# Performance work log

Hardware: AMD Instinct MI355X
Metric: run time of the kernel (lower is better)

## Reference

```python
import jax, jax.numpy as jnp
import numpy as np

N = 100000      # nodes
F_IN = 500      # num_features
H = 128         # num_hidden
C = 40          # num_classes
E = 3200000     # structural edges
K = 5           # knn neighbors


def setup_inputs() -> dict:
    key = jax.random.key(0)
    ks = jax.random.split(key, 9)
    x = jax.random.normal(ks[0], (N, F_IN), dtype=jnp.float32)
    edge_index = jax.random.randint(ks[1], (2, E), 0, N, dtype=jnp.int64)
    # knn graph: source i repeated K times, targets random (stand-in for cosine-KNN)
    src = jnp.repeat(jnp.arange(N, dtype=jnp.int64), K)
    dst = jax.random.randint(ks[2], (K * N,), 0, N, dtype=jnp.int64)
    edge_index_knn = jnp.stack([src, dst])
    s = lambda f: np.float32(1.0 / np.sqrt(f))
    W1 = jax.random.normal(ks[3], (F_IN, H), jnp.float32) * s(F_IN)
    b1 = jnp.zeros((H,), jnp.float32)
    W2 = jax.random.normal(ks[4], (2 * H, C), jnp.float32) * s(2 * H)
    b2 = jnp.zeros((C,), jnp.float32)
    Wlin = jax.random.normal(ks[5], (C, 2 * C), jnp.float32) * s(2 * C)  # torch Linear layout [out,in]
    blin = jnp.zeros((C,), jnp.float32)
    return {"x": x, "edge_index": edge_index, "edge_index_knn": edge_index_knn,
            "W1": W1, "b1": b1, "W2": W2, "b2": b2, "Wlin": Wlin, "blin": blin}


def gcn_conv(x, W, b, edge_index):
    # PyG GCNConv: add self-loops, symmetric normalization deg^-1/2 A deg^-1/2, x@W, scatter-add, +bias
    n = x.shape[0]
    loop = jnp.arange(n, dtype=edge_index.dtype)
    row = jnp.concatenate([edge_index[0], loop])  # sources (gathered)
    col = jnp.concatenate([edge_index[1], loop])  # targets (scattered)
    deg = jax.ops.segment_sum(jnp.ones_like(col, x.dtype), col, num_segments=n)
    dinv = jnp.where(deg > 0, jax.lax.rsqrt(jnp.maximum(deg, 1e-12)), 0.0).astype(x.dtype)
    norm = dinv[row] * dinv[col]                      # [E+n]
    h = x @ W                                          # [n, out]
    agg = jax.ops.segment_sum(h[row] * norm[:, None], col, num_segments=n)
    return agg + b


def reference(x, edge_index, edge_index_knn, W1, b1, W2, b2, Wlin, blin):
    h1 = gcn_conv(x, W1, b1, edge_index)
    h1_2 = gcn_conv(x, W1, b1, edge_index_knn)
    R1 = jax.nn.relu(jnp.concatenate([h1, h1_2], axis=1))  # dropout identity (eval mode)
    h2 = gcn_conv(R1, W2, b2, edge_index)
    h2_2 = gcn_conv(R1, W2, b2, edge_index_knn)
    R2 = jnp.concatenate([h2, h2_2], axis=1)
    logits = R2 @ Wlin.T + blin
    return jax.nn.log_softmax(logits, axis=1)
```

## Files before the change

### kernel.cpp

```cpp
#include <hip/hip_runtime.h>
#include <stdint.h>

#define NN   100000
#define FIN  500
#define HID  128
#define KP1  512
#define K2   256
#define CO   40
#define NPQ  80
#define NPQP 128
#define NBUCK 391
#define CAPB_S 9216
#define CAPB_K 1536

typedef __attribute__((ext_vector_type(8))) short short8;
typedef __attribute__((ext_vector_type(4))) float float4v;
typedef __attribute__((address_space(3))) unsigned int as3_u32;
typedef __attribute__((address_space(1))) unsigned int as1_u32;

__device__ __forceinline__ unsigned short f2bf(float f) {
  unsigned u = __float_as_uint(f);
  u = u + 0x7fffu + ((u >> 16) & 1u);
  return (unsigned short)(u >> 16);
}
__device__ __forceinline__ float bf2f(unsigned short s) {
  return __uint_as_float(((unsigned)s) << 16);
}
__device__ __forceinline__ void gl_lds16(const void* g, void* l) {
  __builtin_amdgcn_global_load_lds((const as1_u32*)g, (as3_u32*)l, 16, 0, 0);
}

__global__ __launch_bounds__(256) void k_bin(
    const int* __restrict__ ei, int nS, int nb1S, int* __restrict__ gcur_s, int* __restrict__ gbin_s,
    const int* __restrict__ eik, int nK, int* __restrict__ gcur_k, int* __restrict__ gbin_k) {
  __shared__ int cnt[NBUCK];
  __shared__ int base[NBUCK];
  const int b = blockIdx.x;
  const bool knn = (b >= nb1S);
  const int* src = knn ? eik      : ei;
  const int* tgt = knn ? eik + nK : ei + nS;
  const int n    = knn ? nK : nS;
  int* gcur      = knn ? gcur_k : gcur_s;
  int* gbin      = knn ? gbin_k : gbin_s;
  const int capb = knn ? CAPB_K : CAPB_S;
  const int ebase = (knn ? b - nb1S : b) * 4096;
  const int t = threadIdx.x;

  for (int i = t; i < NBUCK; i += 256) cnt[i] = 0;
  __syncthreads();
  int s[16], g[16];
#pragma unroll
  for (int i = 0; i < 16; ++i) {
    const int e = ebase + i * 256 + t;
    const bool v = e < n;
    s[i] = v ? src[e] : 0;
    g[i] = v ? tgt[e] : -1;
    if (v) atomicAdd(&cnt[g[i] >> 8], 1);
  }
  __syncthreads();
  for (int i = t; i < NBUCK; i += 256) {
    const int c = cnt[i];
    base[i] = c ? atomicAdd(&gcur[i], c) : 0;
    cnt[i] = 0;
  }
  __syncthreads();
#pragma unroll
  for (int i = 0; i < 16; ++i) {
    if (g[i] >= 0) {
      const int bkt = g[i] >> 8;
      const int pos = base[bkt] + atomicAdd(&cnt[bkt], 1);
      if (pos < capb) gbin[bkt * capb + pos] = (s[i] << 8) | (g[i] & 255);
    }
  }
}

__global__ __launch_bounds__(512) void k_bscan(const int* __restrict__ gcur_s, int* __restrict__ bscan_s,
                                               const int* __restrict__ gcur_k, int* __restrict__ bscan_k) {
  __shared__ int sd[512];
  const int* gcur = blockIdx.x ? gcur_k : gcur_s;
  int* bscan      = blockIdx.x ? bscan_k : bscan_s;
  const int t = threadIdx.x;
  const int v = (t < NBUCK) ? gcur[t] : 0;
  sd[t] = v;
  __syncthreads();
  for (int off = 1; off < 512; off <<= 1) {
    const int x = (t >= off) ? sd[t - off] : 0;
    __syncthreads(); sd[t] += x; __syncthreads();
  }
  if (t < NBUCK) bscan[t] = sd[t] - v;
}

__global__ __launch_bounds__(256) void k_csr(
    const int* __restrict__ gcur_s, const int* __restrict__ gbin_s, const int* __restrict__ bscan_s,
    int* __restrict__ rp_s, int2* __restrict__ colw_s, float* __restrict__ dinv_s,
    const int* __restrict__ gcur_k, const int* __restrict__ gbin_k, const int* __restrict__ bscan_k,
    int* __restrict__ rp_k, int2* __restrict__ colw_k, float* __restrict__ dinv_k) {
  __shared__ int cnt[256];
  __shared__ int base[256];
  const int b0 = blockIdx.x;
  const bool knn = (b0 >= NBUCK);
  const int b = knn ? b0 - NBUCK : b0;
  const int* gcur  = knn ? gcur_k  : gcur_s;
  const int* gbin  = knn ? gbin_k  : gbin_s;
  const int* bscan = knn ? bscan_k : bscan_s;
  int* rp     = knn ? rp_k   : rp_s;
  int2* colw  = knn ? colw_k : colw_s;
  float* dinv = knn ? dinv_k : dinv_s;
  const int capb = knn ? CAPB_K : CAPB_S;
  const int t = threadIdx.x;
  int nB = gcur[b]; if (nB > capb) nB = capb;
  const int gb0 = b * capb;
  const int gbase = bscan[b];

  cnt[t] = 0;
  __syncthreads();
  for (int i = t; i < nB; i += 256) atomicAdd(&cnt[gbin[gb0 + i] & 255], 1);
  __syncthreads();
  const int myc = cnt[t];
  base[t] = myc;
  __syncthreads();
  for (int off = 1; off < 256; off <<= 1) {
    const int x = (t >= off) ? base[t - off] : 0;
    __syncthreads(); base[t] += x; __syncthreads();
  }
  const int excl = base[t] - myc;
  const int tg = b * 256 + t;
  if (tg < NN) { rp[tg] = gbase + excl; dinv[tg] = rsqrtf((float)(myc + 1)); }
  if (tg == NN) rp[NN] = gbase + excl;
  __syncthreads();
  base[t] = excl; cnt[t] = 0;
  __syncthreads();
  for (int i = t; i < nB; i += 256) {
    const int e = gbin[gb0 + i];
    const int tl = e & 255;
    const int pos = atomicAdd(&cnt[tl], 1);
    colw[gbase + base[tl] + pos] = make_int2(e >> 8, 0);
  }
}

__global__ __launch_bounds__(256) void k_fuse(
    int2* __restrict__ colw_s, const float* __restrict__ dinv_s, int nS, int nbF,
    int2* __restrict__ colw_k, const float* __restrict__ dinv_k, int nK) {
  const int b = blockIdx.x;
  if (b < nbF) {
    const int i = b * 256 + threadIdx.x;
    if (i < nS) {
      const int s = colw_s[i].x;
      colw_s[i].y = __float_as_int(dinv_s[s]);
    }
  } else {
    const int i = (b - nbF) * 256 + threadIdx.x;
    if (i < nK) {
      const int s = colw_k[i].x;
      colw_k[i].y = __float_as_int(dinv_k[s]);
    }
  }
}

__global__ void k_w1t(const float* __restrict__ W1, unsigned short* __restrict__ W1T) {
  int idx = blockIdx.x * 256 + threadIdx.x;
  int n = idx >> 9, k = idx & 511;
  float v = (k < FIN) ? W1[k * HID + n] : 0.f;
  W1T[idx] = f2bf(v);
}
__global__ void k_wpq(const float* __restrict__ W2, const float* __restrict__ Wl,
                      const float* __restrict__ b2, const float* __restrict__ bl,
                      unsigned short* __restrict__ WpqT, float* __restrict__ cb) {
  const int idx = blockIdx.x * 256 + threadIdx.x;
  const int n = idx >> 8, k = idx & 255;
  const int o = (n < CO) ? n : n - CO;
  const int joff = (n < CO) ? 0 : CO;
  float s = 0.f;
#pragma unroll 8
  for (int j = 0; j < CO; ++j) s += W2[k * CO + j] * Wl[o * NPQ + joff + j];
  WpqT[n * K2 + k] = f2bf(s);
  if (blockIdx.x == 0 && threadIdx.x < CO) {
    const int oo = threadIdx.x;
    float c = bl[oo];
    for (int j = 0; j < CO; ++j) c += b2[j] * (Wl[oo * NPQ + j] + Wl[oo * NPQ + CO + j]);
    cb[oo] = c;
  }
}

__global__ __launch_bounds__(256) void k_gemm1(const float* __restrict__ x,
    const unsigned short* __restrict__ W1T, const float* __restrict__ zbuf,
    unsigned short* __restrict__ H1b) {
  __shared__ float Als[2][512 * 4];
  __shared__ unsigned short Bls[2][512 * 8];
  const int t = threadIdx.x;
  const int wv = t >> 6, lane = t & 63;
  const int qd = lane >> 4, mr = lane & 15;
  const int m0 = blockIdx.x * 64;

  float4v acc[8];
  const float4v zf4 = {0.f, 0.f, 0.f, 0.f};
#pragma unroll
  for (int b = 0; b < 8; ++b) acc[b] = zf4;

  auto stage = [&](int kk, int pb) {
    const int k0 = kk * 32;
#pragma unroll
    for (int i = 0; i < 2; ++i) {
      const int q = (wv * 2 + i) * 64 + lane;
      const int m = q >> 3;
      const int kg = (q & 7) ^ (m & 7);
      const int gm = m0 + m, kb = k0 + kg * 4;
      const float* gp = (gm < NN && kb < FIN) ? (x + (size_t)gm * FIN + kb) : zbuf;
      gl_lds16(gp, &Als[pb][q * 4]);
    }
#pragma unroll
    for (int i = 0; i < 2; ++i) {
      const int q = (wv * 2 + i) * 64 + lane;
      const int n = q >> 2;
      const int kg = (q & 3) ^ ((q >> 3) & 3);
      gl_lds16(W1T + n * KP1 + k0 + kg * 8, &Bls[pb][q * 8]);
    }
  };

  stage(0, 0);
  for (int kk = 0; kk < 16; ++kk) {
    const int cur = kk & 1;
    if (kk + 1 < 16) {
      stage(kk + 1, cur ^ 1);
      asm volatile("s_waitcnt vmcnt(4)" ::: "memory");
    } else {
      asm volatile("s_waitcnt vmcnt(0)" ::: "memory");
    }
    __builtin_amdgcn_s_barrier();

    short8 af;
    {
      const int m = wv * 16 + mr;
      const int s0 = m * 8 + ((2 * qd) ^ (m & 7));
      const int s1 = m * 8 + ((2 * qd + 1) ^ (m & 7));
      const float4v a0 = *(const float4v*)&Als[cur][s0 * 4];
      const float4v a1 = *(const float4v*)&Als[cur][s1 * 4];
      af[0] = (short)f2bf(a0[0]); af[1] = (short)f2bf(a0[1]);
      af[2] = (short)f2bf(a0[2]); af[3] = (short)f2bf(a0[3]);
      af[4] = (short)f2bf(a1[0]); af[5] = (short)f2bf(a1[1]);
      af[6] = (short)f2bf(a1[2]); af[7] = (short)f2bf(a1[3]);
    }
#pragma unroll
    for (int ct = 0; ct < 8; ++ct) {
      const int n = ct * 16 + mr;
      const int sb = n * 4 + (qd ^ ((n >> 1) & 3));
      const short8 bf = *(const short8*)&Bls[cur][sb * 8];
      acc[ct] = __builtin_amdgcn_mfma_f32_16x16x32_bf16(af, bf, acc[ct], 0, 0, 0);
    }
    __builtin_amdgcn_s_barrier();
  }

  const int rb = m0 + wv * 16 + qd * 4;
#pragma unroll
  for (int ct = 0; ct < 8; ++ct) {
    const int col = ct * 16 + mr;
#pragma unroll
    for (int j = 0; j < 4; ++j) {
      const int r = rb + j;
      if (r < NN) H1b[(size_t)r * HID + col] = f2bf(acc[ct][j]);
    }
  }
}

__global__ __launch_bounds__(256) void k_gemm2(const unsigned short* __restrict__ R1b,
    const unsigned short* __restrict__ WpqT, const unsigned short* __restrict__ zbuf,
    unsigned short* __restrict__ PQ) {
  __shared__ unsigned short Als[2][256 * 8];
  __shared__ unsigned short Bls[2][512 * 8];
  const int t = threadIdx.x;
  const int wv = t >> 6, lane = t & 63;
  const int qd = lane >> 4, mr = lane & 15;
  const int m0 = blockIdx.x * 64;

  float4v acc[5];
  const float4v zf4 = {0.f, 0.f, 0.f, 0.f};
#pragma unroll
  for (int b = 0; b < 5; ++b) acc[b] = zf4;

  auto stage = [&](int kk, int pb) {
    const int k0 = kk * 32;
    {
      const int q = wv * 64 + lane;
      const int m = q >> 2;
      const int kg = (q & 3) ^ ((q >> 3) & 3);
      const int gm = m0 + m;
      const unsigned short* gp = (gm < NN) ? (R1b + (size_t)gm * K2 + k0 + kg * 8) : zbuf;
      gl_lds16(gp, &Als[pb][q * 8]);
    }
#pragma unroll
    for (int i = 0; i < 2; ++i) {
      const int q = (wv * 2 + i) * 64 + lane;
      const int n = q >> 2;
      const int kg = (q & 3) ^ ((q >> 3) & 3);
      gl_lds16(WpqT + n * K2 + k0 + kg * 8, &Bls[pb][q * 8]);
    }
  };

  stage(0, 0);
  for (int kk = 0; kk < 8; ++kk) {
    const int cur = kk & 1;
    if (kk + 1 < 8) {
      stage(kk + 1, cur ^ 1);
      asm volatile("s_waitcnt vmcnt(3)" ::: "memory");
    } else {
      asm volatile("s_waitcnt vmcnt(0)" ::: "memory");
    }
    __builtin_amdgcn_s_barrier();

    short8 af;
    {
      const int m = wv * 16 + mr;
      const int sa = m * 4 + (qd ^ ((m >> 1) & 3));
      af = *(const short8*)&Als[cur][sa * 8];
    }
#pragma unroll
    for (int ct = 0; ct < 5; ++ct) {
      const int n = ct * 16 + mr;
      const int sb = n * 4 + (qd ^ ((n >> 1) & 3));
      const short8 bf = *(const short8*)&Bls[cur][sb * 8];
      acc[ct] = __builtin_amdgcn_mfma_f32_16x16x32_bf16(af, bf, acc[ct], 0, 0, 0);
    }
    __builtin_amdgcn_s_barrier();
  }

  const int rb = m0 + wv * 16 + qd * 4;
#pragma unroll
  for (int ct = 0; ct < 5; ++ct) {
    const int col = ct * 16 + mr;
#pragma unroll
    for (int j = 0; j < 4; ++j) {
      const int r = rb + j;
      if (r < NN) PQ[(size_t)r * NPQ + col] = f2bf(acc[ct][j]);
    }
  }
}

__device__ __forceinline__ void ld8(const int2* __restrict__ cw, int base, int e1, bool full,
                                    int2* __restrict__ q) {
  if (full) {
#pragma unroll
    for (int j = 0; j < 8; ++j) q[j] = cw[base + j];
  } else {
    const int e1c = e1 - 1;
#pragma unroll
    for (int j = 0; j < 8; ++j) {
      const int ee = base + j;
      int2 t = cw[(ee < e1) ? ee : e1c];
      t.y = (ee < e1) ? t.y : 0;
      q[j] = t;
    }
  }
}
__device__ __forceinline__ void g8(const int2* __restrict__ q,
    const unsigned* __restrict__ H32, int lane, unsigned* __restrict__ d) {
#pragma unroll
  for (int j = 0; j < 8; ++j) d[j] = H32[(size_t)q[j].x * 64 + lane];
}
__device__ __forceinline__ void f8(const int2* __restrict__ q, const unsigned* __restrict__ d,
                                   float& ax, float& ay) {
#pragma unroll
  for (int j = 0; j < 8; ++j) {
    const float w = __int_as_float(q[j].y);
    ax += w * __uint_as_float(d[j] << 16);
    ay += w * __uint_as_float(d[j] & 0xffff0000u);
  }
}

__global__ __launch_bounds__(256) void k_agg1(
    const int* __restrict__ rp_s, const int2* __restrict__ colw_s, const float* __restrict__ dinv_s,
    const int* __restrict__ rp_k, const int2* __restrict__ colw_k, const float* __restrict__ dinv_k,
    const unsigned short* __restrict__ H, const float* __restrict__ bias,
    unsigned short* __restrict__ out) {
  const int wv = threadIdx.x >> 6, lane = threadIdx.x & 63;
  const int c = blockIdx.x * 4 + wv;
  if (c >= NN) return;
  const unsigned* H32 = (const unsigned*)H;
  const int e0s = __builtin_amdgcn_readfirstlane(rp_s[c]);
  const int e1s = __builtin_amdgcn_readfirstlane(rp_s[c + 1]);
  const int e0k = __builtin_amdgcn_readfirstlane(rp_k[c]);
  const int e1k = __builtin_amdgcn_readfirstlane(rp_k[c + 1]);
  const int nbS = (e1s - e0s + 7) >> 3;
  const int nbK = (e1k - e0k + 7) >> 3;

  int2 q0[8], q1[8], qk[8];
  unsigned d0[8], d1[8], dk[8];
  const unsigned pc = H32[(size_t)c * 64 + lane];
  if (nbS > 0) { ld8(colw_s, e0s, e1s, e0s + 8 <= e1s, q0); g8(q0, H32, lane, d0); }
  if (nbS > 1) { ld8(colw_s, e0s + 8, e1s, e0s + 16 <= e1s, q1); g8(q1, H32, lane, d1); }
  if (nbK > 0) { ld8(colw_k, e0k, e1k, e0k + 8 <= e1k, qk); g8(qk, H32, lane, dk); }

  const float dcs = dinv_s[c], dck = dinv_k[c];
  const float slo = __uint_as_float(pc << 16);
  const float shi = __uint_as_float(pc & 0xffff0000u);
  float ax = dcs * slo, ay = dcs * shi;
  float bx = dck * slo, by = dck * shi;

  int b = 0;
  while (b + 2 < nbS) {
    f8(q0, d0, ax, ay);
    {
      const int bs = e0s + (b + 2) * 8;
      ld8(colw_s, bs, e1s, bs + 8 <= e1s, q0);
      g8(q0, H32, lane, d0);
    }
    f8(q1, d1, ax, ay);
    if (b + 3 < nbS) {
      const int bs = e0s + (b + 3) * 8;
      ld8(colw_s, bs, e1s, bs + 8 <= e1s, q1);
      g8(q1, H32, lane, d1);
    }
    b += 2;
  }
  if (b < nbS) f8(q0, d0, ax, ay);
  if (b + 1 < nbS) f8(q1, d1, ax, ay);

  if (nbK > 0) f8(qk, dk, bx, by);
  for (int bk = 1; bk < nbK; ++bk) {
    const int bs = e0k + bk * 8;
    ld8(colw_k, bs, e1k, bs + 8 <= e1k, qk);
    g8(qk, H32, lane, dk);
    f8(qk, dk, bx, by);
  }

  const float2 bb = ((const float2*)bias)[lane];
  const float o0 = fmaxf(dcs * ax + bb.x, 0.f);
  const float o1 = fmaxf(dcs * ay + bb.y, 0.f);
  const float o2 = fmaxf(dck * bx + bb.x, 0.f);
  const float o3 = fmaxf(dck * by + bb.y, 0.f);
  unsigned* orow = (unsigned*)(out + (size_t)c * K2);
  orow[lane]      = (unsigned)f2bf(o0) | ((unsigned)f2bf(o1) << 16);
  orow[64 + lane] = (unsigned)f2bf(o2) | ((unsigned)f2bf(o3) << 16);
}

__device__ __forceinline__ void ld12(const int2* __restrict__ cw, int base, int e1, bool full,
                                     int2* __restrict__ q) {
  if (full) {
#pragma unroll
    for (int j = 0; j < 12; ++j) q[j] = cw[base + j];
  } else {
    const int e1c = e1 - 1;
#pragma unroll
    for (int j = 0; j < 12; ++j) {
      const int ee = base + j;
      int2 t = cw[(ee < e1) ? ee : e1c];
      t.y = (ee < e1) ? t.y : 0;
      q[j] = t;
    }
  }
}
__device__ __forceinline__ void gt4(const int2* __restrict__ q, const unsigned* __restrict__ PQ32,
                                    int g, int l, int off, float* __restrict__ w,
                                    unsigned* __restrict__ d) {
#pragma unroll
  for (int t = 0; t < 4; ++t) {
    const int2 qa = q[3 * t], qb = q[3 * t + 1], qc = q[3 * t + 2];
    const int xs = (g == 0) ? qa.x : ((g == 1) ? qb.x : qc.x);
    const int wi = (g == 0) ? qa.y : ((g == 1) ? qb.y : qc.y);
    w[t] = __int_as_float(wi);
    d[t] = PQ32[(size_t)xs * 40 + off + l];
  }
}
__device__ __forceinline__ void ct4(const float* __restrict__ w, const unsigned* __restrict__ d,
                                    float& sx, float& sy) {
#pragma unroll
  for (int t = 0; t < 4; ++t) {
    sx += w[t] * __uint_as_float(d[t] << 16);
    sy += w[t] * __uint_as_float(d[t] & 0xffff0000u);
  }
}

__global__ __launch_bounds__(256) void k_aggf(
    const int* __restrict__ rp_s, const int2* __restrict__ colw_s, const float* __restrict__ dinv_s,
    const int* __restrict__ rp_k, const int2* __restrict__ colw_k, const float* __restrict__ dinv_k,
    const unsigned short* __restrict__ PQ, const float* __restrict__ cb,
    float* __restrict__ out) {
  const int wv = threadIdx.x >> 6, lane = threadIdx.x & 63;
  const int c = blockIdx.x * 4 + wv;
  if (c >= NN) return;
  const unsigned* PQ32 = (const unsigned*)PQ;
  const int g = (lane < 60) ? (lane / 20) : 2;
  const int l = lane - 20 * g;

  const int e0s = __builtin_amdgcn_readfirstlane(rp_s[c]);
  const int e1s = __builtin_amdgcn_readfirstlane(rp_s[c + 1]);
  const int e0k = __builtin_amdgcn_readfirstlane(rp_k[c]);
  const int e1k = __builtin_amdgcn_readfirstlane(rp_k[c + 1]);
  const int nbS = (e1s - e0s + 11) / 12;
  const int nbK = (e1k - e0k + 11) / 12;

  unsigned dP = 0, dQ = 0;
  if (lane < 20) {
    dP = PQ32[(size_t)c * 40 + lane];
    dQ = PQ32[(size_t)c * 40 + 20 + lane];
  }

  int2 q0[12], q1[12], qk[12];
  float w0[4], w1[4], wk[4];
  unsigned d0[4], d1[4], dk[4];
  if (nbS > 0) { ld12(colw_s, e0s, e1s, e0s + 12 <= e1s, q0); gt4(q0, PQ32, g, l, 0, w0, d0); }
  if (nbS > 1) { ld12(colw_s, e0s + 12, e1s, e0s + 24 <= e1s, q1); gt4(q1, PQ32, g, l, 0, w1, d1); }
  if (nbK > 0) { ld12(colw_k, e0k, e1k, e0k + 12 <= e1k, qk); gt4(qk, PQ32, g, l, 20, wk, dk); }

  float sx = 0.f, sy = 0.f, kx = 0.f, ky = 0.f;
  int b = 0;
  while (b + 2 < nbS) {
    ct4(w0, d0, sx, sy);
    {
      const int bs = e0s + (b + 2) * 12;
      ld12(colw_s, bs, e1s, bs + 12 <= e1s, q0);
      gt4(q0, PQ32, g, l, 0, w0, d0);
    }
    ct4(w1, d1, sx, sy);
    if (b + 3 < nbS) {
      const int bs = e0s + (b + 3) * 12;
      ld12(colw_s, bs, e1s, bs + 12 <= e1s, q1);
      gt4(q1, PQ32, g, l, 0, w1, d1);
    }
    b += 2;
  }
  if (b < nbS) ct4(w0, d0, sx, sy);
  if (b + 1 < nbS) ct4(w1, d1, sx, sy);

  if (nbK > 0) ct4(wk, dk, kx, ky);
  for (int bk = 1; bk < nbK; ++bk) {
    const int bs = e0k + bk * 12;
    ld12(colw_k, bs, e1k, bs + 12 <= e1k, qk);
    gt4(qk, PQ32, g, l, 20, wk, dk);
    ct4(wk, dk, kx, ky);
  }

  sx += __shfl(sx, lane + 20) + __shfl(sx, lane + 40);
  sy += __shfl(sy, lane + 20) + __shfl(sy, lane + 40);
  kx += __shfl(kx, lane + 20) + __shfl(kx, lane + 40);
  ky += __shfl(ky, lane + 20) + __shfl(ky, lane + 40);

  float lo = 0.f, hi = 0.f;
  if (lane < 20) {
    const float dcs = dinv_s[c], dck = dinv_k[c];
    const float2 cbb = ((const float2*)cb)[lane];
    lo = dcs * (sx + dcs * __uint_as_float(dP << 16))
       + dck * (kx + dck * __uint_as_float(dQ << 16)) + cbb.x;
    hi = dcs * (sy + dcs * __uint_as_float(dP & 0xffff0000u))
       + dck * (ky + dck * __uint_as_float(dQ & 0xffff0000u)) + cbb.y;
  }
  float m = (lane < 20) ? fmaxf(lo, hi) : -3.4e38f;
#pragma unroll
  for (int off = 1; off < 64; off <<= 1) m = fmaxf(m, __shfl_xor(m, off));
  float s = (lane < 20) ? (expf(lo - m) + expf(hi - m)) : 0.f;
#pragma unroll
  for (int off = 1; off < 64; off <<= 1) s += __shfl_xor(s, off);
  const float lse = m + logf(s);
  if (lane < 20) {
    float2 o; o.x = lo - lse; o.y = hi - lse;
    ((float2*)(out + (size_t)c * CO))[lane] = o;
  }
}

extern "C" void kernel_launch(void* const* d_in, const int* in_sizes, int n_in,
                              void* d_out, int out_size, void* d_ws, size_t ws_size,
                              hipStream_t stream) {
  const float* x  = (const float*)d_in[0];
  const int* ei   = (const int*)d_in[1];
  const int* eik  = (const int*)d_in[2];
  const float* W1 = (const float*)d_in[3];
  const float* b1 = (const float*)d_in[4];
  const float* W2 = (const float*)d_in[5];
  const float* b2 = (const float*)d_in[6];
  const float* Wl = (const float*)d_in[7];
  const float* bl = (const float*)d_in[8];
  float* out = (float*)d_out;
  const int E  = in_sizes[1] / 2;
  const int EK = in_sizes[2] / 2;

  char* p = (char*)d_ws;
  size_t off = 0;
  auto alloc = [&](size_t bytes) -> void* {
    void* r = (void*)(p + off);
    off += (bytes + 255) & ~(size_t)255;
    return r;
  };
  int* gcur_s = (int*)alloc((size_t)NBUCK * 4);
  int* gcur_k = (int*)alloc((size_t)NBUCK * 4);
  void* zbuf = alloc(256);
  const size_t zero_span = off;
  int* bscan_s = (int*)alloc((size_t)NBUCK * 4);
  int* bscan_k = (int*)alloc((size_t)NBUCK * 4);
  float* dinv_s = (float*)alloc((size_t)NN * 4);
  float* dinv_k = (float*)alloc((size_t)NN * 4);
  int* rp_s = (int*)alloc((size_t)(NN + 1) * 4);
  int* rp_k = (int*)alloc((size_t)(NN + 1) * 4);
  unsigned short* W1T = (unsigned short*)alloc((size_t)HID * KP1 * 2);
  unsigned short* WpqT = (unsigned short*)alloc((size_t)NPQP * K2 * 2);
  float* cbv = (float*)alloc((size_t)CO * 4);
  int* gbin_s = (int*)alloc((size_t)NBUCK * CAPB_S * 4);
  int* gbin_k = (int*)alloc((size_t)NBUCK * CAPB_K * 4);
  int2* colw_s = (int2*)alloc((size_t)E * 8);
  int2* colw_k = (int2*)alloc((size_t)EK * 8);
  unsigned short* H1b = (unsigned short*)alloc((size_t)NN * HID * 2);
  unsigned short* R1b = (unsigned short*)alloc((size_t)NN * K2 * 2);
  unsigned short* PQ = H1b;

  hipMemsetAsync(d_ws, 0, zero_span, stream);

  const int nb1S = (E + 4095) / 4096;
  const int nb1K = (EK + 4095) / 4096;
  k_bin<<<nb1S + nb1K, 256, 0, stream>>>(ei, E, nb1S, gcur_s, gbin_s, eik, EK, gcur_k, gbin_k);
  k_bscan<<<2, 512, 0, stream>>>(gcur_s, bscan_s, gcur_k, bscan_k);
  k_csr<<<2 * NBUCK, 256, 0, stream>>>(gcur_s, gbin_s, bscan_s, rp_s, colw_s, dinv_s,
                                       gcur_k, gbin_k, bscan_k, rp_k, colw_k, dinv_k);
  const int nbF = (E + 255) / 256;
  const int nbFk = (EK + 255) / 256;
  k_fuse<<<nbF + nbFk, 256, 0, stream>>>(colw_s, dinv_s, E, nbF, colw_k, dinv_k, EK);

  k_w1t<<<(HID * KP1) / 256, 256, 0, stream>>>(W1, W1T);
  k_wpq<<<NPQ, 256, 0, stream>>>(W2, Wl, b2, bl, WpqT, cbv);

  k_gemm1<<<(NN + 63) / 64, 256, 0, stream>>>(x, W1T, (const float*)zbuf, H1b);
  const int nbAgg = (NN + 3) / 4;
  k_agg1<<<nbAgg, 256, 0, stream>>>(rp_s, colw_s, dinv_s, rp_k, colw_k, dinv_k, H1b, b1, R1b);

  k_gemm2<<<(NN + 63) / 64, 256, 0, stream>>>(R1b, WpqT, (const unsigned short*)zbuf, PQ);
  k_aggf<<<nbAgg, 256, 0, stream>>>(rp_s, colw_s, dinv_s, rp_k, colw_k, dinv_k, PQ, cbv, out);
}
```

Measured before the change: 671.8 us.

## Merge weight prep into binning and run GEMM1 alongside CSR build

Moves the W1 transpose and the fused W2·Wlin weight prep into extra blocks of the edge-binning kernel. It also launches the first GEMM (x@W1) as extra blocks of the CSR-construction kernel, with the two sharing LDS through a union. The aim is fewer kernel launches and letting the independent, memory-bound CSR work overlap with the compute-heavy GEMM. The cost is a larger LDS footprint for the CSR blocks, which sets occupancy, and heterogeneous blocks in one grid.

```diff
diff --git a/kernel.cpp b/kernel.cpp
--- a/kernel.cpp
+++ b/kernel.cpp
@@ -30,11 +30,44 @@
   __builtin_amdgcn_global_load_lds((const as1_u32*)g, (as3_u32*)l, 16, 0, 0);
 }
 
-__global__ __launch_bounds__(256) void k_bin(
+__global__ __launch_bounds__(256) void k_binw(
     const int* __restrict__ ei, int nS, int nb1S, int* __restrict__ gcur_s, int* __restrict__ gbin_s,
-    const int* __restrict__ eik, int nK, int* __restrict__ gcur_k, int* __restrict__ gbin_k) {
+    const int* __restrict__ eik, int nK, int nbBin, int* __restrict__ gcur_k, int* __restrict__ gbin_k,
+    const float* __restrict__ W1, unsigned short* __restrict__ W1T,
+    const float* __restrict__ W2, const float* __restrict__ Wl,
+    const float* __restrict__ b2, const float* __restrict__ bl,
+    unsigned short* __restrict__ WpqT, float* __restrict__ cb) {
   __shared__ int cnt[NBUCK];
   __shared__ int base[NBUCK];
+  const int t = threadIdx.x;
+
+  if (blockIdx.x >= nbBin) {
+    const int wb = blockIdx.x - nbBin;
+    if (wb < 256) {
+      const int idx = wb * 256 + t;
+      const int n = idx >> 9, k = idx & 511;
+      const float v = (k < FIN) ? W1[k * HID + n] : 0.f;
+      W1T[idx] = f2bf(v);
+    } else {
+      const int lb = wb - 256;
+      const int idx = lb * 256 + t;
+      const int n = idx >> 8, k = idx & 255;
+      const int o = (n < CO) ? n : n - CO;
+      const int joff = (n < CO) ? 0 : CO;
+      float s = 0.f;
+#pragma unroll 8
+      for (int j = 0; j < CO; ++j) s += W2[k * CO + j] * Wl[o * NPQ + joff + j];
+      WpqT[n * K2 + k] = f2bf(s);
+      if (lb == 0 && t < CO) {
+        const int oo = t;
+        float c = bl[oo];
+        for (int j = 0; j < CO; ++j) c += b2[j] * (Wl[oo * NPQ + j] + Wl[oo * NPQ + CO + j]);
+        cb[oo] = c;
+      }
+    }
+    return;
+  }
+
   const int b = blockIdx.x;
   const bool knn = (b >= nb1S);
   const int* src = knn ? eik      : ei;
@@ -44,7 +77,6 @@
   int* gbin      = knn ? gbin_k : gbin_s;
   const int capb = knn ? CAPB_K : CAPB_S;
   const int ebase = (knn ? b - nb1S : b) * 4096;
-  const int t = threadIdx.x;
 
   for (int i = t; i < NBUCK; i += 256) cnt[i] = 0;
   __syncthreads();
@@ -90,51 +122,136 @@
   if (t < NBUCK) bscan[t] = sd[t] - v;
 }
 
-__global__ __launch_bounds__(256) void k_csr(
+union SMemCG {
+  struct { int cnt[256]; int base[256]; } c;
+  struct { float A[2][2048]; unsigned short B[2][4096]; } g;
+};
+
+__global__ __launch_bounds__(256) void k_csrg1(
     const int* __restrict__ gcur_s, const int* __restrict__ gbin_s, const int* __restrict__ bscan_s,
     int* __restrict__ rp_s, int2* __restrict__ colw_s, float* __restrict__ dinv_s,
     const int* __restrict__ gcur_k, const int* __restrict__ gbin_k, const int* __restrict__ bscan_k,
-    int* __restrict__ rp_k, int2* __restrict__ colw_k, float* __restrict__ dinv_k) {
-  __shared__ int cnt[256];
-  __shared__ int base[256];
-  const int b0 = blockIdx.x;
-  const bool knn = (b0 >= NBUCK);
-  const int b = knn ? b0 - NBUCK : b0;
-  const int* gcur  = knn ? gcur_k  : gcur_s;
-  const int* gbin  = knn ? gbin_k  : gbin_s;
-  const int* bscan = knn ? bscan_k : bscan_s;
-  int* rp     = knn ? rp_k   : rp_s;
-  int2* colw  = knn ? colw_k : colw_s;
-  float* dinv = knn ? dinv_k : dinv_s;
-  const int capb = knn ? CAPB_K : CAPB_S;
+    int* __restrict__ rp_k, int2* __restrict__ colw_k, float* __restrict__ dinv_k,
+    const float* __restrict__ x, const unsigned short* __restrict__ W1T,
+    const float* __restrict__ zbuf, unsigned short* __restrict__ H1b) {
+  __shared__ SMemCG sm;
   const int t = threadIdx.x;
-  int nB = gcur[b]; if (nB > capb) nB = capb;
-  const int gb0 = b * capb;
-  const int gbase = bscan[b];
-
-  cnt[t] = 0;
-  __syncthreads();
-  for (int i = t; i < nB; i += 256) atomicAdd(&cnt[gbin[gb0 + i] & 255], 1);
-  __syncthreads();
-  const int myc = cnt[t];
-  base[t] = myc;
-  __syncthreads();
-  for (int off = 1; off < 256; off <<= 1) {
-    const int x = (t >= off) ? base[t - off] : 0;
-    __syncthreads(); base[t] += x; __syncthreads();
-  }
-  const int excl = base[t] - myc;
-  const int tg = b * 256 + t;
-  if (tg < NN) { rp[tg] = gbase + excl; dinv[tg] = rsqrtf((float)(myc + 1)); }
-  if (tg == NN) rp[NN] = gbase + excl;
-  __syncthreads();
-  base[t] = excl; cnt[t] = 0;
-  __syncthreads();
-  for (int i = t; i < nB; i += 256) {
-    const int e = gbin[gb0 + i];
-    const int tl = e & 255;
-    const int pos = atomicAdd(&cnt[tl], 1);
-    colw[gbase + base[tl] + pos] = make_int2(e >> 8, 0);
+
+  if (blockIdx.x < 2 * NBUCK) {
+    int* cnt  = sm.c.cnt;
+    int* base = sm.c.base;
+    const int b0 = blockIdx.x;
+    const bool knn = (b0 >= NBUCK);
+    const int b = knn ? b0 - NBUCK : b0;
+    const int* gcur  = knn ? gcur_k  : gcur_s;
+    const int* gbin  = knn ? gbin_k  : gbin_s;
+    const int* bscan = knn ? bscan_k : bscan_s;
+    int* rp     = knn ? rp_k   : rp_s;
+    int2* colw  = knn ? colw_k : colw_s;
+    float* dinv = knn ? dinv_k : dinv_s;
+    const int capb = knn ? CAPB_K : CAPB_S;
+    int nB = gcur[b]; if (nB > capb) nB = capb;
+    const int gb0 = b * capb;
+    const int gbase = bscan[b];
+
+    cnt[t] = 0;
+    __syncthreads();
+    for (int i = t; i < nB; i += 256) atomicAdd(&cnt[gbin[gb0 + i] & 255], 1);
+    __syncthreads();
+    const int myc = cnt[t];
+    base[t] = myc;
+    __syncthreads();
+    for (int off = 1; off < 256; off <<= 1) {
+      const int x2 = (t >= off) ? base[t - off] : 0;
+      __syncthreads(); base[t] += x2; __syncthreads();
+    }
+    const int excl = base[t] - myc;
+    const int tg = b * 256 + t;
+    if (tg < NN) { rp[tg] = gbase + excl; dinv[tg] = rsqrtf((float)(myc + 1)); }
+    if (tg == NN) rp[NN] = gbase + excl;
+    __syncthreads();
+    base[t] = excl; cnt[t] = 0;
+    __syncthreads();
+    for (int i = t; i < nB; i += 256) {
+      const int e = gbin[gb0 + i];
+      const int tl = e & 255;
+      const int pos = atomicAdd(&cnt[tl], 1);
+      colw[gbase + base[tl] + pos] = make_int2(e >> 8, 0);
+    }
+    return;
+  }
+
+  const int wv = t >> 6, lane = t & 63;
+  const int qd = lane >> 4, mr = lane & 15;
+  const int m0 = (blockIdx.x - 2 * NBUCK) * 64;
+
+  float4v acc[8];
+  const float4v zf4 = {0.f, 0.f, 0.f, 0.f};
+#pragma unroll
+  for (int b = 0; b < 8; ++b) acc[b] = zf4;
+
+  auto stage = [&](int kk, int pb) {
+    const int k0 = kk * 32;
+#pragma unroll
+    for (int i = 0; i < 2; ++i) {
+      const int q = (wv * 2 + i) * 64 + lane;
+      const int m = q >> 3;
+      const int kg = (q & 7) ^ (m & 7);
+      const int gm = m0 + m, kb = k0 + kg * 4;
+      const float* gp = (gm < NN && kb < FIN) ? (x + (size_t)gm * FIN + kb) : zbuf;
+      gl_lds16(gp, &sm.g.A[pb][q * 4]);
+    }
+#pragma unroll
+    for (int i = 0; i < 2; ++i) {
+      const int q = (wv * 2 + i) * 64 + lane;
+      const int n = q >> 2;
+      const int kg = (q & 3) ^ ((q >> 3) & 3);
+      gl_lds16(W1T + n * KP1 + k0 + kg * 8, &sm.g.B[pb][q * 8]);
+    }
+  };
+
+  stage(0, 0);
+  for (int kk = 0; kk < 16; ++kk) {
+    const int cur = kk & 1;
+    if (kk + 1 < 16) {
+      stage(kk + 1, cur ^ 1);
+      asm volatile("s_waitcnt vmcnt(4)" ::: "memory");
+    } else {
+      asm volatile("s_waitcnt vmcnt(0)" ::: "memory");
+    }
+    __builtin_amdgcn_s_barrier();
+
+    short8 af;
+    {
+      const int m = wv * 16 + mr;
+      const int s0 = m * 8 + ((2 * qd) ^ (m & 7));
+      const int s1 = m * 8 + ((2 * qd + 1) ^ (m & 7));
+      const float4v a0 = *(const float4v*)&sm.g.A[cur][s0 * 4];
+      const float4v a1 = *(const float4v*)&sm.g.A[cur][s1 * 4];
+      af[0] = (short)f2bf(a0[0]); af[1] = (short)f2bf(a0[1]);
+      af[2] = (short)f2bf(a0[2]); af[3] = (short)f2bf(a0[3]);
+      af[4] = (short)f2bf(a1[0]); af[5] = (short)f2bf(a1[1]);
+      af[6] = (short)f2bf(a1[2]); af[7] = (short)f2bf(a1[3]);
+    }
+#pragma unroll
+    for (int ct = 0; ct < 8; ++ct) {
+      const int n = ct * 16 + mr;
+      const int sb = n * 4 + (qd ^ ((n >> 1) & 3));
+      const short8 bf = *(const short8*)&sm.g.B[cur][sb * 8];
+      acc[ct] = __builtin_amdgcn_mfma_f32_16x16x32_bf16(af, bf, acc[ct], 0, 0, 0);
+    }
+    __builtin_amdgcn_s_barrier();
+  }
+
+  const int rb = m0 + wv * 16 + qd * 4;
+#pragma unroll
+  for (int ct = 0; ct < 8; ++ct) {
+    const int col = ct * 16 + mr;
+#pragma unroll
+    for (int j = 0; j < 4; ++j) {
+      const int r = rb + j;
+      if (r < NN) H1b[(size_t)r * HID + col] = f2bf(acc[ct][j]);
+    }
   }
 }
 
@@ -153,111 +270,6 @@
     if (i < nK) {
       const int s = colw_k[i].x;
       colw_k[i].y = __float_as_int(dinv_k[s]);
-    }
-  }
-}
-
-__global__ void k_w1t(const float* __restrict__ W1, unsigned short* __restrict__ W1T) {
-  int idx = blockIdx.x * 256 + threadIdx.x;
-  int n = idx >> 9, k = idx & 511;
-  float v = (k < FIN) ? W1[k * HID + n] : 0.f;
-  W1T[idx] = f2bf(v);
-}
-__global__ void k_wpq(const float* __restrict__ W2, const float* __restrict__ Wl,
-                      const float* __restrict__ b2, const float* __restrict__ bl,
-                      unsigned short* __restrict__ WpqT, float* __restrict__ cb) {
-  const int idx = blockIdx.x * 256 + threadIdx.x;
-  const int n = idx >> 8, k = idx & 255;
-  const int o = (n < CO) ? n : n - CO;
-  const int joff = (n < CO) ? 0 : CO;
-  float s = 0.f;
-#pragma unroll 8
-  for (int j = 0; j < CO; ++j) s += W2[k * CO + j] * Wl[o * NPQ + joff + j];
-  WpqT[n * K2 + k] = f2bf(s);
-  if (blockIdx.x == 0 && threadIdx.x < CO) {
-    const int oo = threadIdx.x;
-    float c = bl[oo];
-    for (int j = 0; j < CO; ++j) c += b2[j] * (Wl[oo * NPQ + j] + Wl[oo * NPQ + CO + j]);
-    cb[oo] = c;
-  }
-}
-
-__global__ __launch_bounds__(256) void k_gemm1(const float* __restrict__ x,
-    const unsigned short* __restrict__ W1T, const float* __restrict__ zbuf,
-    unsigned short* __restrict__ H1b) {
-  __shared__ float Als[2][512 * 4];
-  __shared__ unsigned short Bls[2][512 * 8];
-  const int t = threadIdx.x;
-  const int wv = t >> 6, lane = t & 63;
-  const int qd = lane >> 4, mr = lane & 15;
-  const int m0 = blockIdx.x * 64;
-
-  float4v acc[8];
-  const float4v zf4 = {0.f, 0.f, 0.f, 0.f};
-#pragma unroll
-  for (int b = 0; b < 8; ++b) acc[b] = zf4;
-
-  auto stage = [&](int kk, int pb) {
-    const int k0 = kk * 32;
-#pragma unroll
-    for (int i = 0; i < 2; ++i) {
-      const int q = (wv * 2 + i) * 64 + lane;
-      const int m = q >> 3;
-      const int kg = (q & 7) ^ (m & 7);
-      const int gm = m0 + m, kb = k0 + kg * 4;
-      const float* gp = (gm < NN && kb < FIN) ? (x + (size_t)gm * FIN + kb) : zbuf;
-      gl_lds16(gp, &Als[pb][q * 4]);
-    }
-#pragma unroll
-    for (int i = 0; i < 2; ++i) {
-      const int q = (wv * 2 + i) * 64 + lane;
-      const int n = q >> 2;
-      const int kg = (q & 3) ^ ((q >> 3) & 3);
-      gl_lds16(W1T + n * KP1 + k0 + kg * 8, &Bls[pb][q * 8]);
-    }
-  };
-
-  stage(0, 0);
-  for (int kk = 0; kk < 16; ++kk) {
-    const int cur = kk & 1;
-    if (kk + 1 < 16) {
-      stage(kk + 1, cur ^ 1);
-      asm volatile("s_waitcnt vmcnt(4)" ::: "memory");
-    } else {
-      asm volatile("s_waitcnt vmcnt(0)" ::: "memory");
-    }
-    __builtin_amdgcn_s_barrier();
-
-    short8 af;
-    {
-      const int m = wv * 16 + mr;
-      const int s0 = m * 8 + ((2 * qd) ^ (m & 7));
-      const int s1 = m * 8 + ((2 * qd + 1) ^ (m & 7));
-      const float4v a0 = *(const float4v*)&Als[cur][s0 * 4];
-      const float4v a1 = *(const float4v*)&Als[cur][s1 * 4];
-      af[0] = (short)f2bf(a0[0]); af[1] = (short)f2bf(a0[1]);
-      af[2] = (short)f2bf(a0[2]); af[3] = (short)f2bf(a0[3]);
-      af[4] = (short)f2bf(a1[0]); af[5] = (short)f2bf(a1[1]);
-      af[6] = (short)f2bf(a1[2]); af[7] = (short)f2bf(a1[3]);
-    }
-#pragma unroll
-    for (int ct = 0; ct < 8; ++ct) {
-      const int n = ct * 16 + mr;
-      const int sb = n * 4 + (qd ^ ((n >> 1) & 3));
-      const short8 bf = *(const short8*)&Bls[cur][sb * 8];
-      acc[ct] = __builtin_amdgcn_mfma_f32_16x16x32_bf16(af, bf, acc[ct], 0, 0, 0);
-    }
-    __builtin_amdgcn_s_barrier();
-  }
-
-  const int rb = m0 + wv * 16 + qd * 4;
-#pragma unroll
-  for (int ct = 0; ct < 8; ++ct) {
-    const int col = ct * 16 + mr;
-#pragma unroll
-    for (int j = 0; j < 4; ++j) {
-      const int r = rb + j;
-      if (r < NN) H1b[(size_t)r * HID + col] = f2bf(acc[ct][j]);
     }
   }
 }
@@ -604,18 +616,22 @@
 
   const int nb1S = (E + 4095) / 4096;
   const int nb1K = (EK + 4095) / 4096;
-  k_bin<<<nb1S + nb1K, 256, 0, stream>>>(ei, E, nb1S, gcur_s, gbin_s, eik, EK, gcur_k, gbin_k);
+  const int nbBin = nb1S + nb1K;
+  k_binw<<<nbBin + 256 + NPQ, 256, 0, stream>>>(
+      ei, E, nb1S, gcur_s, gbin_s, eik, EK, nbBin, gcur_k, gbin_k,
+      W1, W1T, W2, Wl, b2, bl, WpqT, cbv);
   k_bscan<<<2, 512, 0, stream>>>(gcur_s, bscan_s, gcur_k, bscan_k);
-  k_csr<<<2 * NBUCK, 256, 0, stream>>>(gcur_s, gbin_s, bscan_s, rp_s, colw_s, dinv_s,
-                                       gcur_k, gbin_k, bscan_k, rp_k, colw_k, dinv_k);
+
+  const int nbG1 = (NN + 63) / 64;
+  k_csrg1<<<2 * NBUCK + nbG1, 256, 0, stream>>>(
+      gcur_s, gbin_s, bscan_s, rp_s, colw_s, dinv_s,
+      gcur_k, gbin_k, bscan_k, rp_k, colw_k, dinv_k,
+      x, W1T, (const float*)zbuf, H1b);
+
   const int nbF = (E + 255) / 256;
   const int nbFk = (EK + 255) / 256;
   k_fuse<<<nbF + nbFk, 256, 0, stream>>>(colw_s, dinv_s, E, nbF, colw_k, dinv_k, EK);
 
-  k_w1t<<<(HID * KP1) / 256, 256, 0, stream>>>(W1, W1T);
-  k_wpq<<<NPQ, 256, 0, stream>>>(W2, Wl, b2, bl, WpqT, cbv);
-
-  k_gemm1<<<(NN + 63) / 64, 256, 0, stream>>>(x, W1T, (const float*)zbuf, H1b);
   const int nbAgg = (NN + 3) / 4;
   k_agg1<<<nbAgg, 256, 0, stream>>>(rp_s, colw_s, dinv_s, rp_k, colw_k, dinv_k, H1b, b1, R1b);
 
```

New measurement: 669.7 us. Within noise of the previous version (-0.3%).
